# Kernel optimization log

Hardware: AMD Instinct MI355X
Metric: run time of the kernel (lower is better)

The kernel has to match this reference:

```python
import jax, jax.numpy as jnp
import numpy as np

B = 1048576
C = 64


def setup_inputs() -> dict:
    key = jax.random.key(0)
    k1, k2 = jax.random.split(key)
    pred = jax.random.normal(k1, (B, C), dtype=jnp.float32)
    target = jax.random.randint(k2, (B,), 0, C, dtype=jnp.int64)
    return {"pred": pred, "target": target, "num_classes": C}


def _build_target_probs(target, num_classes):
    """Vectorized, faithful port of FilteredCrossEntropyLoss.apply_filter."""
    Cc = num_classes
    Bb = target.shape[0]
    f32 = jnp.float32
    # Edge filters (full length C, zero-padded like the torch constants).
    left = jnp.zeros((Cc,), f32).at[:3].set(jnp.array([0.6, 0.25, 0.15], f32))
    mid_left = jnp.zeros((Cc,), f32).at[:4].set(jnp.array([0.25, 0.4, 0.25, 0.1], f32))
    mid_right = jnp.zeros((Cc,), f32).at[-4:].set(jnp.array([0.1, 0.25, 0.4, 0.25], f32))
    right = jnp.zeros((Cc,), f32).at[-3:].set(jnp.array([0.15, 0.25, 0.6], f32))
    filt_else = jnp.array([0.1, 0.23, 0.34, 0.23, 0.1], f32)
    # 'else' branch: torch places filt_else at [padding, padding+5) then
    # torch.roll by (t - 2) with wraparound; element j lands at
    # (padding + j + t - 2) mod C. Replicate exactly (including wraparound).
    padding = (Cc - 5) // 2
    idx = (padding + target[:, None] - 2 + jnp.arange(5)) % Cc  # [B, 5]
    tp_else = jnp.zeros((Bb, Cc), f32).at[jnp.arange(Bb)[:, None], idx].set(
        jnp.broadcast_to(filt_else, (Bb, 5))
    )
    # Select per-row filter by target position.
    mask_left = (target == 0)[:, None]
    mask_mid_left = (target == 1)[:, None]
    mask_mid_right = (target == Cc - 2)[:, None]
    mask_right = (target == Cc - 1)[:, None]
    tp = jnp.where(mask_left, left,
         jnp.where(mask_mid_left, mid_left,
         jnp.where(mask_mid_right, mid_right,
         jnp.where(mask_right, right, tp_else))))
    return tp


def reference(pred, target, num_classes):
    tp = _build_target_probs(target, num_classes)  # [B, C]
    logp = jax.nn.log_softmax(pred, axis=1)
    # torch KLDivLoss(reduction='batchmean'): sum(t*(log t - logp) where t>0) / B
    pointwise = jnp.where(tp > 0, tp * (jnp.log(jnp.where(tp > 0, tp, 1.0)) - logp), 0.0)
    return jnp.sum(pointwise) / pred.shape[0]
```

## Files before the change

### kernel.cpp

```cpp
#include <hip/hip_runtime.h>
#include <math.h>


#define THREADS 256
#define NBLOCKS 2048

__device__ __forceinline__ float dpp_add16(float x) {
    int v;
    v = __builtin_amdgcn_update_dpp(0, __float_as_int(x), 0xB1,  0xF, 0xF, true);
    x += __int_as_float(v);
    v = __builtin_amdgcn_update_dpp(0, __float_as_int(x), 0x4E,  0xF, 0xF, true);
    x += __int_as_float(v);
    v = __builtin_amdgcn_update_dpp(0, __float_as_int(x), 0x141, 0xF, 0xF, true);
    x += __int_as_float(v);
    v = __builtin_amdgcn_update_dpp(0, __float_as_int(x), 0x140, 0xF, 0xF, true);
    x += __int_as_float(v);
    return x;
}

__global__ __launch_bounds__(THREADS, 8)
void fce_main(const float* __restrict__ pred, const int* __restrict__ target,
              float* __restrict__ partial, int ngroups,
              float K0, float K1, float Ke) {
    const int tid  = threadIdx.x;
    const int lane = tid & 63;
    const int wid  = tid >> 6;
    const int sub  = lane >> 4;
    const int gw   = blockIdx.x * 4 + wid;
    const int nw   = gridDim.x * 4;

    float acc = 0.0f;

    for (int g = gw; g < ngroups; g += nw) {
        const int row = g * 4 + sub;
        const float4 p4 = *reinterpret_cast<const float4*>(
            pred + (size_t)g * 256 + (size_t)lane * 4);
        const int t = target[row];

        float es = __expf(p4.x) + __expf(p4.y) + __expf(p4.z) + __expf(p4.w);
        es = dpp_add16(es);
        const float lse = __logf(es);

        const bool e0 = (t == 0), e1 = (t == 1), e62 = (t == 62), e63 = (t == 63);
        const bool edge = e0 | e1 | e62 | e63;
        const int  b  = edge ? ((e0 | e1) ? 0 : (e62 ? 60 : 61)) : ((t + 27) & 63);
        const float f0 = e0 ? .60f : e1 ? .25f : e62 ? .10f : e63 ? .15f : .10f;
        const float f1 = e0 ? .25f : e1 ? .40f : e62 ? .25f : e63 ? .25f : .23f;
        const float f2 = e0 ? .15f : e1 ? .25f : e62 ? .40f : e63 ? .60f : .34f;
        const float f3 = e1 ? .10f : e62 ? .25f : (edge ? 0.0f : .23f);
        const float f4 = edge ? 0.0f : .10f;

        const float* rp = pred + (size_t)row * 64;
        const float wp = f0 * rp[b]
                       + f1 * rp[(b + 1) & 63]
                       + f2 * rp[(b + 2) & 63]
                       + f3 * rp[(b + 3) & 63]
                       + f4 * rp[(b + 4) & 63];

        const float Kc = (e0 | e63) ? K0 : ((e1 | e62) ? K1 : Ke);
        acc += Kc + lse - wp;
    }

    acc += __shfl_xor(acc, 16);
    acc += __shfl_xor(acc, 32);

    __shared__ float sred[4];
    if (lane == 0) sred[wid] = acc;
    __syncthreads();
    if (tid == 0)
        partial[blockIdx.x] = sred[0] + sred[1] + sred[2] + sred[3];
}

__global__ __launch_bounds__(THREADS)
void fce_reduce(const float* __restrict__ partial, int n,
                float* __restrict__ out, float invB) {
    float s = 0.0f;
    for (int i = threadIdx.x; i < n; i += THREADS) s += partial[i];
    #pragma unroll
    for (int m = 1; m < 64; m <<= 1) s += __shfl_xor(s, m);
    __shared__ float ws[4];
    const int wid = threadIdx.x >> 6;
    if ((threadIdx.x & 63) == 0) ws[wid] = s;
    __syncthreads();
    if (threadIdx.x == 0)
        out[0] = (ws[0] + ws[1] + ws[2] + ws[3]) * invB;
}

extern "C" void kernel_launch(void* const* d_in, const int* in_sizes, int n_in,
                              void* d_out, int out_size, void* d_ws, size_t ws_size,
                              hipStream_t stream) {
    const float* pred  = (const float*)d_in[0];
    const int* target  = (const int*)d_in[1];
    float* partial     = (float*)d_ws;
    float* out         = (float*)d_out;

    const int B = in_sizes[1];
    const int ngroups = B / 4;

    const float K0 = 0.60f * logf(0.60f) + 0.25f * logf(0.25f) + 0.15f * logf(0.15f);
    const float K1 = 0.25f * logf(0.25f) + 0.40f * logf(0.40f)
                   + 0.25f * logf(0.25f) + 0.10f * logf(0.10f);
    const float Ke = 2.0f * 0.10f * logf(0.10f) + 2.0f * 0.23f * logf(0.23f)
                   + 0.34f * logf(0.34f);

    fce_main<<<NBLOCKS, THREADS, 0, stream>>>(pred, target, partial, ngroups,
                                              K0, K1, Ke);
    fce_reduce<<<1, THREADS, 0, stream>>>(partial, NBLOCKS, out, 1.0f / (float)B);
}
```

Baseline: 58.40 us.

## Fuse final reduction via atomics, compute filter weights in-register, process two rows per lane

Replaces the separate reduce kernel with a last-block-done pattern using fixed-point 64-bit atomic accumulation and a completion counter, which needs a memset of the workspace first. The five scattered gather loads of pred per row are replaced by weights computed directly from each lane's own four columns, with a wave-uniform branch for the edge targets. Each lane now handles two rows per iteration using nontemporal vector loads for pred and for pairs of targets. This aims to cut the second launch and the redundant gather traffic, at the cost of fixed-point quantization of the block sums and an added memset node.

```diff
diff --git a/kernel.cpp b/kernel.cpp
--- a/kernel.cpp
+++ b/kernel.cpp
@@ -4,6 +4,10 @@
 
 #define THREADS 256
 #define NBLOCKS 2048
+#define RPI 8
+
+typedef float  f32x4 __attribute__((ext_vector_type(4)));
+typedef int    i32x2 __attribute__((ext_vector_type(2)));
 
 __device__ __forceinline__ float dpp_add16(float x) {
     int v;
@@ -18,92 +22,116 @@
     return x;
 }
 
+__device__ __forceinline__ float row_term(f32x4 p, int t, int cbase,
+                                          float K0, float K1, float Ke) {
+    float es = __expf(p.x) + __expf(p.y) + __expf(p.z) + __expf(p.w);
+    es = dpp_add16(es);
+    const float lse = __logf(es);
+
+    const int j0 = cbase - t + 37;
+    float w[4], pp[4] = {p.x, p.y, p.z, p.w};
+    #pragma unroll
+    for (int k = 0; k < 4; ++k) {
+        const int j = (j0 + k) & 63;
+        const float d = fabsf((float)(j - 2));
+        w[k] = fmaxf(0.0f, __fmaf_rn(d, __fmaf_rn(d, -0.01f, -0.10f), 0.34f));
+    }
+    float K = Ke;
+    const bool edge = (t < 2) | (t >= 62);
+    if (__any(edge)) {
+        const bool mir = (t >= 62);
+        const int  tt  = mir ? 63 - t : t;
+        const float a0 = tt ? 0.25f : 0.60f;
+        const float a1 = tt ? 0.40f : 0.25f;
+        const float a2 = tt ? 0.25f : 0.15f;
+        const float a3 = tt ? 0.10f : 0.00f;
+        #pragma unroll
+        for (int k = 0; k < 4; ++k) {
+            const int cc = mir ? 63 - (cbase + k) : (cbase + k);
+            const float we = (cc == 0) ? a0 : (cc == 1) ? a1
+                           : (cc == 2) ? a2 : (cc == 3) ? a3 : 0.0f;
+            if (edge) w[k] = we;
+        }
+        if (edge) K = tt ? K1 : K0;
+    }
+    float wp = 0.0f;
+    #pragma unroll
+    for (int k = 0; k < 4; ++k) wp = __fmaf_rn(w[k], pp[k], wp);
+    return __fmaf_rn(K + lse, 0.0625f, -wp);
+}
+
 __global__ __launch_bounds__(THREADS, 8)
 void fce_main(const float* __restrict__ pred, const int* __restrict__ target,
-              float* __restrict__ partial, int ngroups,
-              float K0, float K1, float Ke) {
-    const int tid  = threadIdx.x;
-    const int lane = tid & 63;
-    const int wid  = tid >> 6;
-    const int sub  = lane >> 4;
-    const int gw   = blockIdx.x * 4 + wid;
-    const int nw   = gridDim.x * 4;
+              unsigned int* __restrict__ counter,
+              unsigned long long* __restrict__ gsum,
+              float* __restrict__ out, int ngroups,
+              float K0, float K1, float Ke, double outscale) {
+    const int tid   = threadIdx.x;
+    const int lane  = tid & 63;
+    const int wid   = tid >> 6;
+    const int s     = lane >> 4;
+    const int cbase = (lane & 15) * 4;
+    const int gw    = blockIdx.x * 4 + wid;
+    const int nw    = gridDim.x * 4;
 
     float acc = 0.0f;
 
     for (int g = gw; g < ngroups; g += nw) {
-        const int row = g * 4 + sub;
-        const float4 p4 = *reinterpret_cast<const float4*>(
-            pred + (size_t)g * 256 + (size_t)lane * 4);
-        const int t = target[row];
-
-        float es = __expf(p4.x) + __expf(p4.y) + __expf(p4.z) + __expf(p4.w);
-        es = dpp_add16(es);
-        const float lse = __logf(es);
-
-        const bool e0 = (t == 0), e1 = (t == 1), e62 = (t == 62), e63 = (t == 63);
-        const bool edge = e0 | e1 | e62 | e63;
-        const int  b  = edge ? ((e0 | e1) ? 0 : (e62 ? 60 : 61)) : ((t + 27) & 63);
-        const float f0 = e0 ? .60f : e1 ? .25f : e62 ? .10f : e63 ? .15f : .10f;
-        const float f1 = e0 ? .25f : e1 ? .40f : e62 ? .25f : e63 ? .25f : .23f;
-        const float f2 = e0 ? .15f : e1 ? .25f : e62 ? .40f : e63 ? .60f : .34f;
-        const float f3 = e1 ? .10f : e62 ? .25f : (edge ? 0.0f : .23f);
-        const float f4 = edge ? 0.0f : .10f;
-
-        const float* rp = pred + (size_t)row * 64;
-        const float wp = f0 * rp[b]
-                       + f1 * rp[(b + 1) & 63]
-                       + f2 * rp[(b + 2) & 63]
-                       + f3 * rp[(b + 3) & 63]
-                       + f4 * rp[(b + 4) & 63];
-
-        const float Kc = (e0 | e63) ? K0 : ((e1 | e62) ? K1 : Ke);
-        acc += Kc + lse - wp;
+        const float* base = pred + (size_t)g * (RPI * 64) + (2 * s) * 64 + cbase;
+        const f32x4 a = __builtin_nontemporal_load(
+            reinterpret_cast<const f32x4*>(base));
+        const f32x4 b = __builtin_nontemporal_load(
+            reinterpret_cast<const f32x4*>(base + 64));
+        const i32x2 t2 = __builtin_nontemporal_load(
+            reinterpret_cast<const i32x2*>(target + (size_t)g * RPI + 2 * s));
+        acc += row_term(a, t2.x, cbase, K0, K1, Ke);
+        acc += row_term(b, t2.y, cbase, K0, K1, Ke);
     }
 
-    acc += __shfl_xor(acc, 16);
-    acc += __shfl_xor(acc, 32);
+    #pragma unroll
+    for (int m = 1; m < 64; m <<= 1) acc += __shfl_xor(acc, m);
 
     __shared__ float sred[4];
+    __shared__ int lastflag;
     if (lane == 0) sred[wid] = acc;
     __syncthreads();
-    if (tid == 0)
-        partial[blockIdx.x] = sred[0] + sred[1] + sred[2] + sred[3];
-}
-
-__global__ __launch_bounds__(THREADS)
-void fce_reduce(const float* __restrict__ partial, int n,
-                float* __restrict__ out, float invB) {
-    float s = 0.0f;
-    for (int i = threadIdx.x; i < n; i += THREADS) s += partial[i];
-    #pragma unroll
-    for (int m = 1; m < 64; m <<= 1) s += __shfl_xor(s, m);
-    __shared__ float ws[4];
-    const int wid = threadIdx.x >> 6;
-    if ((threadIdx.x & 63) == 0) ws[wid] = s;
+    if (tid == 0) {
+        const float bsum = sred[0] + sred[1] + sred[2] + sred[3];
+        const long long q = (long long)llrintf(bsum * 274877906944.0f);
+        __hip_atomic_fetch_add(gsum, (unsigned long long)q,
+                               __ATOMIC_RELEASE, __HIP_MEMORY_SCOPE_AGENT);
+        const unsigned int prev = __hip_atomic_fetch_add(
+            counter, 1u, __ATOMIC_ACQ_REL, __HIP_MEMORY_SCOPE_AGENT);
+        lastflag = (prev == (unsigned)(gridDim.x - 1));
+    }
     __syncthreads();
-    if (threadIdx.x == 0)
-        out[0] = (ws[0] + ws[1] + ws[2] + ws[3]) * invB;
+    if (lastflag && tid == 0) {
+        const unsigned long long sv = __hip_atomic_load(
+            gsum, __ATOMIC_ACQUIRE, __HIP_MEMORY_SCOPE_AGENT);
+        out[0] = (float)((double)(long long)sv * outscale);
+    }
 }
 
 extern "C" void kernel_launch(void* const* d_in, const int* in_sizes, int n_in,
                               void* d_out, int out_size, void* d_ws, size_t ws_size,
                               hipStream_t stream) {
-    const float* pred  = (const float*)d_in[0];
-    const int* target  = (const int*)d_in[1];
-    float* partial     = (float*)d_ws;
-    float* out         = (float*)d_out;
+    const float* pred = (const float*)d_in[0];
+    const int* target = (const int*)d_in[1];
+    unsigned int* counter = (unsigned int*)d_ws;
+    unsigned long long* gsum = (unsigned long long*)((char*)d_ws + 8);
+    float* out = (float*)d_out;
 
     const int B = in_sizes[1];
-    const int ngroups = B / 4;
+    const int ngroups = B / RPI;
 
     const float K0 = 0.60f * logf(0.60f) + 0.25f * logf(0.25f) + 0.15f * logf(0.15f);
     const float K1 = 0.25f * logf(0.25f) + 0.40f * logf(0.40f)
                    + 0.25f * logf(0.25f) + 0.10f * logf(0.10f);
     const float Ke = 2.0f * 0.10f * logf(0.10f) + 2.0f * 0.23f * logf(0.23f)
                    + 0.34f * logf(0.34f);
+    const double outscale = 1.0 / (274877906944.0 * (double)B);
 
-    fce_main<<<NBLOCKS, THREADS, 0, stream>>>(pred, target, partial, ngroups,
-                                              K0, K1, Ke);
-    fce_reduce<<<1, THREADS, 0, stream>>>(partial, NBLOCKS, out, 1.0f / (float)B);
+    hipMemsetAsync(d_ws, 0, 16, stream);
+    fce_main<<<NBLOCKS, THREADS, 0, stream>>>(pred, target, counter, gsum, out,
+                                              ngroups, K0, K1, Ke, outscale);
 }
```

Result: slower. 226.7 us (+288.2%).
